# Kernel tuning notes

Measured on AMD Instinct MI355X. Metric: run time of the kernel, lower is better.

## Reference

```python
import jax, jax.numpy as jnp
import numpy as np
import math

B, S, D_MODEL = 4, 2048, 1024
H, D_QK, D_V = 16, 64, 64


def setup_inputs() -> dict:
    key = jax.random.key(0)
    ks = jax.random.split(key, 12)
    s = 0.02
    return {
        "input_q": jax.random.normal(ks[0], (B, S, D_MODEL), jnp.float32),
        "input_k": jax.random.normal(ks[1], (B, S, D_MODEL), jnp.float32),
        "input_v": jax.random.normal(ks[2], (B, S, D_MODEL), jnp.float32),
        # per-head projection weights stacked over heads: [H, out, d_model] (torch Linear layout)
        "WQw": jax.random.normal(ks[3], (H, D_QK, D_MODEL), jnp.float32) * s,
        "WQb": jax.random.normal(ks[4], (H, D_QK), jnp.float32) * s,
        "WKw": jax.random.normal(ks[5], (H, D_QK, D_MODEL), jnp.float32) * s,
        "WKb": jax.random.normal(ks[6], (H, D_QK), jnp.float32) * s,
        "WVw": jax.random.normal(ks[7], (H, D_V, D_MODEL), jnp.float32) * s,
        "WVb": jax.random.normal(ks[8], (H, D_V), jnp.float32) * s,
        # output projection: Linear(H*D_V, D_MODEL)
        "Ww": jax.random.normal(ks[9], (D_MODEL, H * D_V), jnp.float32) * s,
        "Wb": jax.random.normal(ks[10], (D_MODEL,), jnp.float32) * s,
    }


def _mha(input_q, input_k, input_v, WQw, WQb, WKw, WKb, WVw, WVb, Ww, Wb):
    # per-head projections: [B,H,S,d]
    Q = jnp.einsum("bsd,hed->bhse", input_q, WQw) + WQb[None, :, None, :]
    K = jnp.einsum("bsd,hed->bhse", input_k, WKw) + WKb[None, :, None, :]
    V = jnp.einsum("bsd,hvd->bhsv", input_v, WVw) + WVb[None, :, None, :]
    scores = jnp.einsum("bhse,bhte->bhst", Q, K)  # [B,H,S,S]
    # causal mask added BEFORE division by sqrt(d_model), as in original
    causal = jnp.triu(jnp.full((S, S), -jnp.inf, scores.dtype), k=1)
    scores = (scores + causal) / math.sqrt(D_MODEL)  # NOTE: d_model, not d_qk
    attn = jax.nn.softmax(scores, axis=-1)
    ctx = jnp.einsum("bhst,bhtv->bhsv", attn, V)  # [B,H,S,D_V]
    concat = ctx.transpose(0, 2, 1, 3).reshape(B, S, H * D_V)  # head-order concat
    return concat @ Ww.T + Wb


def reference(input_q, input_k, input_v, WQw, WQb, WKw, WKb, WVw, WVb, Ww, Wb):
    return _mha(input_q, input_k, input_v, WQw, WQb, WKw, WKb, WVw, WVb, Ww, Wb)
```

## Files before the change

### kernel.cpp

```cpp
#include <hip/hip_runtime.h>
#include <hip/hip_bf16.h>

typedef __attribute__((ext_vector_type(8))) short bf16x8;
typedef __attribute__((ext_vector_type(4))) short bf16x4;
typedef __attribute__((ext_vector_type(4))) float f32x4;

#define MFMA16(a, b, c) __builtin_amdgcn_mfma_f32_16x16x32_bf16(a, b, c, 0, 0, 0)

__device__ __forceinline__ unsigned short f2bfn(float f) {
#if defined(__gfx950__)
  __bf16 h = (__bf16)f;
  return __builtin_bit_cast(unsigned short, h);
#else
  union { float f; unsigned u; } x; x.f = f;
  unsigned r = x.u + 0x7fffu + ((x.u >> 16) & 1u);
  return (unsigned short)(r >> 16);
#endif
}

__device__ __forceinline__ void cvt_body(const float* __restrict__ s,
                                         unsigned short* __restrict__ d, int n8) {
  int i = blockIdx.x * blockDim.x + threadIdx.x;
  int st = gridDim.x * blockDim.x;
  for (; i < n8; i += st) {
    const float4* sp = reinterpret_cast<const float4*>(s) + 2 * (size_t)i;
    float4 a = sp[0], b = sp[1];
    bf16x8 o;
    o[0] = (short)f2bfn(a.x); o[1] = (short)f2bfn(a.y);
    o[2] = (short)f2bfn(a.z); o[3] = (short)f2bfn(a.w);
    o[4] = (short)f2bfn(b.x); o[5] = (short)f2bfn(b.y);
    o[6] = (short)f2bfn(b.z); o[7] = (short)f2bfn(b.w);
    reinterpret_cast<bf16x8*>(d)[i] = o;
  }
}

__global__ void cvt1_kernel(const float* __restrict__ s, unsigned short* __restrict__ d, int n8) {
  cvt_body(s, d, n8);
}

__global__ void cvt_w_kernel(const float* s0, const float* s1, const float* s2, const float* s3,
                             unsigned short* d0, unsigned short* d1, unsigned short* d2,
                             unsigned short* d3, int n8) {
  const float* s; unsigned short* d;
  switch (blockIdx.y) {
    case 0: s = s0; d = d0; break;
    case 1: s = s1; d = d1; break;
    case 2: s = s2; d = d2; break;
    default: s = s3; d = d3; break;
  }
  cvt_body(s, d, n8);
}

template <int MODE>
__global__ __launch_bounds__(256) void gemm_kernel(
    const unsigned short* __restrict__ Av, const unsigned short* __restrict__ Bv,
    const float* __restrict__ bias, void* __restrict__ outv,
    int M, int N, int K) {
  constexpr int BM = 128, BN = 128, BK = 64;
  __shared__ __align__(16) unsigned short As[2][BM * BK];
  __shared__ __align__(16) unsigned short Bs[2][BN * BK];
  const int tid = threadIdx.x;
  const int lane = tid & 63, wave = tid >> 6;
  const int wr = wave >> 1, wc = wave & 1;
  const int m0 = blockIdx.y * BM, n0 = blockIdx.x * BN;
  const int rb = lane & 15, g = lane >> 4;
  const int swz = ((lane & 7) ^ ((lane >> 3) & 7)) * 8;
  f32x4 acc[4][4] = {};

  const unsigned short* Ab = Av + (size_t)m0 * K;
  const unsigned short* Bb = Bv + (size_t)n0 * K;

  auto stage = [&](int buf, int k0) {
#pragma unroll
    for (int i = 0; i < 4; ++i) {
      const int c = wave * 256 + i * 64 + lane;
      const int r = c >> 3;
      __builtin_amdgcn_global_load_lds(
          (const __attribute__((address_space(1))) unsigned int*)(Ab + (size_t)r * K + k0 + swz),
          (__attribute__((address_space(3))) unsigned int*)&As[buf][c * 8], 16, 0, 0);
      __builtin_amdgcn_global_load_lds(
          (const __attribute__((address_space(1))) unsigned int*)(Bb + (size_t)r * K + k0 + swz),
          (__attribute__((address_space(3))) unsigned int*)&Bs[buf][c * 8], 16, 0, 0);
    }
  };

  const int nt = K / BK;
  stage(0, 0);
  int cur = 0;
  for (int t = 0; t < nt; ++t) {
    __syncthreads();
    if (t + 1 < nt) stage(cur ^ 1, (t + 1) * BK);
    const unsigned short* A_ = As[cur];
    const unsigned short* B_ = Bs[cur];
#pragma unroll
    for (int kc = 0; kc < 2; ++kc) {
      bf16x8 af[4], bfr[4];
#pragma unroll
      for (int mi = 0; mi < 4; ++mi)
        af[mi] = *reinterpret_cast<const bf16x8*>(
            &A_[(wr * 64 + mi * 16 + rb) * 64 + (((kc * 4 + g) ^ (rb & 7)) * 8)]);
#pragma unroll
      for (int ni = 0; ni < 4; ++ni)
        bfr[ni] = *reinterpret_cast<const bf16x8*>(
            &B_[(wc * 64 + ni * 16 + rb) * 64 + (((kc * 4 + g) ^ (rb & 7)) * 8)]);
#pragma unroll
      for (int mi = 0; mi < 4; ++mi)
#pragma unroll
        for (int ni = 0; ni < 4; ++ni)
          acc[mi][ni] = MFMA16(af[mi], bfr[ni], acc[mi][ni]);
    }
    cur ^= 1;
  }

#pragma unroll
  for (int mi = 0; mi < 4; ++mi) {
#pragma unroll
    for (int ni = 0; ni < 4; ++ni) {
      int col = n0 + wc * 64 + ni * 16 + rb;
      if constexpr (MODE != 2) {
        float bv = bias[col];
#pragma unroll
        for (int j = 0; j < 4; ++j) {
          int row = m0 + wr * 64 + mi * 16 + g * 4 + j;
          float v = acc[mi][ni][j] + bv;
          if constexpr (MODE == 0) {
            int b = row >> 11, s = row & 2047;
            int h = col >> 6, e = col & 63;
            ((unsigned short*)outv)[((size_t)(b * 16 + h) * 2048 + s) * 64 + e] = f2bfn(v);
          } else {
            ((float*)outv)[(size_t)row * N + col] = v;
          }
        }
      } else {
        int bb = col >> 11, s = col & 2047;
#pragma unroll
        for (int j = 0; j < 4; ++j) {
          int row = m0 + wr * 64 + mi * 16 + g * 4 + j;
          float v = acc[mi][ni][j] + bias[row];
          int h = row >> 6, e = row & 63;
          ((unsigned short*)outv)[((size_t)(bb * 16 + h) * 64 + e) * 2048 + s] = f2bfn(v);
        }
      }
    }
  }
}

__global__ __launch_bounds__(256) void attn2_kernel(
    const unsigned short* __restrict__ Qp, const unsigned short* __restrict__ Kp,
    const unsigned short* __restrict__ Vtp, unsigned short* __restrict__ ctx) {
  constexpr int S = 2048;
  __shared__ __align__(16) unsigned short Ks[2][64 * 64];
  __shared__ __align__(16) unsigned short Vs[2][64 * 64];
  __shared__ __align__(16) unsigned short Pl[4][32 * 64];
  const int bx = blockIdx.x;
  const int bh = bx & 63;
  const int qti = 15 - (bx >> 6);
  const int q0 = qti * 128;
  const int tid = threadIdx.x, wave = tid >> 6, lane = tid & 63;
  const int q15 = lane & 15, g = lane >> 4;
  const int qw = q0 + wave * 32;
  const unsigned short* Qb = Qp + (size_t)bh * S * 64;
  const unsigned short* Kb = Kp + (size_t)bh * S * 64;
  const unsigned short* Vb = Vtp + (size_t)bh * 64 * S;

  bf16x8 qf[2][2];
#pragma unroll
  for (int ni = 0; ni < 2; ++ni)
#pragma unroll
    for (int kc = 0; kc < 2; ++kc)
      qf[ni][kc] = *reinterpret_cast<const bf16x8*>(
          Qb + (size_t)(qw + 16 * ni + q15) * 64 + 32 * kc + 8 * g);

  float m2[2] = {-1e30f, -1e30f}, nm2[2] = {0.f, 0.f}, lsum[2] = {0.f, 0.f};
  f32x4 o[4][2] = {};
  const float sc = 0.03125f * 1.4426950408889634f;
  const float TH = 8.0f / sc;
  const int xsw = (q15 & 7);
  const int sswz = ((lane & 7) ^ (lane >> 3)) * 8;
  const int nt = qti * 2 + 2;

  auto stage = [&](int buf, int kv0) {
#pragma unroll
    for (int i = 0; i < 2; ++i) {
      const int ci = (wave * 2 + i) * 64 + lane;
      const int r = (wave * 2 + i) * 8 + (lane >> 3);
      const unsigned short* ksrc = Kb + (size_t)(kv0 + r) * 64 + sswz;
      __builtin_amdgcn_global_load_lds(
          (const __attribute__((address_space(1))) unsigned int*)ksrc,
          (__attribute__((address_space(3))) unsigned int*)&Ks[buf][ci * 8], 16, 0, 0);
      const unsigned short* vsrc = Vb + (size_t)r * S + kv0 + sswz;
      __builtin_amdgcn_global_load_lds(
          (const __attribute__((address_space(1))) unsigned int*)vsrc,
          (__attribute__((address_space(3))) unsigned int*)&Vs[buf][ci * 8], 16, 0, 0);
    }
  };

  stage(0, 0);

  for (int it = 0; it < nt; ++it) {
    __syncthreads();
    if (it + 1 < nt) stage((it + 1) & 1, 64 * (it + 1));
    const int kv0 = 64 * it;
    if (kv0 <= qw + 31) {
      const unsigned short* K_ = Ks[it & 1];
      const unsigned short* V_ = Vs[it & 1];
      f32x4 sacc[4][2] = {};
      __builtin_amdgcn_s_setprio(1);
#pragma unroll
      for (int kc = 0; kc < 2; ++kc) {
#pragma unroll
        for (int mi = 0; mi < 4; ++mi) {
          bf16x8 kf = *reinterpret_cast<const bf16x8*>(
              &K_[(16 * mi + q15) * 64 + ((4 * kc + g) ^ xsw) * 8]);
          sacc[mi][0] = MFMA16(kf, qf[0][kc], sacc[mi][0]);
          sacc[mi][1] = MFMA16(kf, qf[1][kc], sacc[mi][1]);
        }
      }
      __builtin_amdgcn_s_setprio(0);
      if (kv0 + 63 > qw) {
#pragma unroll
        for (int mi = 0; mi < 4; ++mi)
#pragma unroll
          for (int ni = 0; ni < 2; ++ni)
#pragma unroll
            for (int j = 0; j < 4; ++j)
              if (kv0 + 16 * mi + 4 * g + j > qw + 16 * ni + q15) sacc[mi][ni][j] = -1e30f;
      }
      float mt[2] = {-1e30f, -1e30f};
#pragma unroll
      for (int mi = 0; mi < 4; ++mi)
#pragma unroll
        for (int ni = 0; ni < 2; ++ni)
#pragma unroll
          for (int j = 0; j < 4; ++j) mt[ni] = fmaxf(mt[ni], sacc[mi][ni][j]);
#pragma unroll
      for (int ni = 0; ni < 2; ++ni) {
        mt[ni] = fmaxf(mt[ni], __shfl_xor(mt[ni], 16, 64));
        mt[ni] = fmaxf(mt[ni], __shfl_xor(mt[ni], 32, 64));
      }
      bool need = (mt[0] > m2[0] + TH) || (mt[1] > m2[1] + TH);
      if (__any((int)need)) {
#pragma unroll
        for (int ni = 0; ni < 2; ++ni) {
          float mn = fmaxf(m2[ni], mt[ni]);
          float corr = __builtin_amdgcn_exp2f((m2[ni] - mn) * sc);
          m2[ni] = mn;
          nm2[ni] = -mn * sc;
          lsum[ni] *= corr;
#pragma unroll
          for (int mi = 0; mi < 4; ++mi)
#pragma unroll
            for (int j = 0; j < 4; ++j) o[mi][ni][j] *= corr;
        }
      }
      float rs[2] = {0.f, 0.f};
#pragma unroll
      for (int mi = 0; mi < 4; ++mi)
#pragma unroll
        for (int ni = 0; ni < 2; ++ni) {
          bf16x4 pk;
#pragma unroll
          for (int j = 0; j < 4; ++j) {
            float p = __builtin_amdgcn_exp2f(fmaf(sacc[mi][ni][j], sc, nm2[ni]));
            rs[ni] += p;
            pk[j] = (short)f2bfn(p);
          }
          *reinterpret_cast<bf16x4*>(
              &Pl[wave][(q15 + 16 * ni) * 64 +
                        ((2 * mi + (g >> 1)) ^ xsw) * 8 + 4 * (g & 1)]) = pk;
        }
#pragma unroll
      for (int ni = 0; ni < 2; ++ni) {
        rs[ni] += __shfl_xor(rs[ni], 16, 64);
        rs[ni] += __shfl_xor(rs[ni], 32, 64);
        lsum[ni] += rs[ni];
      }
      __builtin_amdgcn_s_setprio(1);
#pragma unroll
      for (int kc = 0; kc < 2; ++kc) {
        bf16x8 pf[2];
#pragma unroll
        for (int ni = 0; ni < 2; ++ni)
          pf[ni] = *reinterpret_cast<const bf16x8*>(
              &Pl[wave][(q15 + 16 * ni) * 64 + ((4 * kc + g) ^ xsw) * 8]);
#pragma unroll
        for (int mi = 0; mi < 4; ++mi) {
          bf16x8 vf = *reinterpret_cast<const bf16x8*>(
              &V_[(16 * mi + q15) * 64 + ((4 * kc + g) ^ xsw) * 8]);
          o[mi][0] = MFMA16(vf, pf[0], o[mi][0]);
          o[mi][1] = MFMA16(vf, pf[1], o[mi][1]);
        }
      }
      __builtin_amdgcn_s_setprio(0);
    }
  }

  const int b = bh >> 4, h = bh & 15;
#pragma unroll
  for (int ni = 0; ni < 2; ++ni) {
    float inv = 1.0f / lsum[ni];
    int q = qw + 16 * ni + q15;
#pragma unroll
    for (int mi = 0; mi < 4; ++mi) {
      bf16x4 pk;
#pragma unroll
      for (int j = 0; j < 4; ++j) pk[j] = (short)f2bfn(o[mi][ni][j] * inv);
      *reinterpret_cast<bf16x4*>(
          ctx + ((size_t)(b * 2048 + q) * 1024) + h * 64 + 16 * mi + 4 * g) = pk;
    }
  }
}

extern "C" void kernel_launch(void* const* d_in, const int* in_sizes, int n_in,
                              void* d_out, int out_size, void* d_ws, size_t ws_size,
                              hipStream_t stream) {
  const float* in_q = (const float*)d_in[0];
  const float* in_k = (const float*)d_in[1];
  const float* in_v = (const float*)d_in[2];
  const float* WQw = (const float*)d_in[3];
  const float* WQb = (const float*)d_in[4];
  const float* WKw = (const float*)d_in[5];
  const float* WKb = (const float*)d_in[6];
  const float* WVw = (const float*)d_in[7];
  const float* WVb = (const float*)d_in[8];
  const float* Ww  = (const float*)d_in[9];
  const float* Wb  = (const float*)d_in[10];
  float* out = (float*)d_out;

  constexpr size_t PROJ = (size_t)4 * 16 * 2048 * 64;
  constexpr size_t WSZ = (size_t)1024 * 1024;
  unsigned short* wsp = (unsigned short*)d_ws;
  unsigned short* Qp   = wsp;
  unsigned short* Kp   = wsp + PROJ;
  unsigned short* Vt   = wsp + 2 * PROJ;
  unsigned short* in16 = wsp + 3 * PROJ;
  unsigned short* ctx  = in16;
  unsigned short* wq16 = wsp + 4 * PROJ;
  unsigned short* wk16 = wq16 + WSZ;
  unsigned short* wv16 = wk16 + WSZ;
  unsigned short* ww16 = wv16 + WSZ;

  cvt_w_kernel<<<dim3(256, 4), 256, 0, stream>>>(WQw, WKw, WVw, Ww,
                                                 wq16, wk16, wv16, ww16, (int)(WSZ / 8));
  cvt1_kernel<<<2048, 256, 0, stream>>>(in_q, in16, (int)(PROJ / 8));
  gemm_kernel<0><<<dim3(8, 64), 256, 0, stream>>>(in16, wq16, WQb, Qp, 8192, 1024, 1024);
  cvt1_kernel<<<2048, 256, 0, stream>>>(in_k, in16, (int)(PROJ / 8));
  gemm_kernel<0><<<dim3(8, 64), 256, 0, stream>>>(in16, wk16, WKb, Kp, 8192, 1024, 1024);
  cvt1_kernel<<<2048, 256, 0, stream>>>(in_v, in16, (int)(PROJ / 8));
  gemm_kernel<2><<<dim3(64, 8), 256, 0, stream>>>(wv16, in16, WVb, Vt, 1024, 8192, 1024);

  attn2_kernel<<<1024, 256, 0, stream>>>(Qp, Kp, Vt, ctx);

  gemm_kernel<1><<<dim3(8, 64), 256, 0, stream>>>(ctx, ww16, Wb, out, 8192, 1024, 1024);
}
```

Before: 196.5 us.

## Switch attention to 32x32 MFMA and keep P in registers via permlane swaps

The attention kernel moves from 16x16x32 to 32x32x16 bf16 MFMA tiles, so each wave computes one 32-query block against two 32-key blocks. The softmax probabilities are packed with v_cvt_pk_bf16_f32 and rearranged into the B-operand layout with permlane32_swap, which removes the per-wave LDS round trip for P. Row max and sum reductions now need only one cross-half shuffle. The cost is more live accumulator registers, which may lower occupancy, and a layout correctness that depends on the permlane mapping.

```diff
diff --git a/kernel.cpp b/kernel.cpp
--- a/kernel.cpp
+++ b/kernel.cpp
@@ -4,8 +4,10 @@
 typedef __attribute__((ext_vector_type(8))) short bf16x8;
 typedef __attribute__((ext_vector_type(4))) short bf16x4;
 typedef __attribute__((ext_vector_type(4))) float f32x4;
+typedef __attribute__((ext_vector_type(16))) float f32x16;
 
 #define MFMA16(a, b, c) __builtin_amdgcn_mfma_f32_16x16x32_bf16(a, b, c, 0, 0, 0)
+#define MFMA32(a, b, c) __builtin_amdgcn_mfma_f32_32x32x16_bf16(a, b, c, 0, 0, 0)
 
 __device__ __forceinline__ unsigned short f2bfn(float f) {
 #if defined(__gfx950__)
@@ -16,6 +18,18 @@
   unsigned r = x.u + 0x7fffu + ((x.u >> 16) & 1u);
   return (unsigned short)(r >> 16);
 #endif
+}
+
+__device__ __forceinline__ void plswap(unsigned& a, unsigned& b) {
+  auto r = __builtin_amdgcn_permlane32_swap(a, b, false, false);
+  a = r[0];
+  b = r[1];
+}
+
+__device__ __forceinline__ unsigned cvtpk(float lo, float hi) {
+  unsigned w;
+  asm("v_cvt_pk_bf16_f32 %0, %1, %2" : "=v"(w) : "v"(lo), "v"(hi));
+  return w;
 }
 
 __device__ __forceinline__ void cvt_body(const float* __restrict__ s,
@@ -145,37 +159,34 @@
   }
 }
 
-__global__ __launch_bounds__(256) void attn2_kernel(
+__global__ __launch_bounds__(256) void attn3_kernel(
     const unsigned short* __restrict__ Qp, const unsigned short* __restrict__ Kp,
     const unsigned short* __restrict__ Vtp, unsigned short* __restrict__ ctx) {
   constexpr int S = 2048;
   __shared__ __align__(16) unsigned short Ks[2][64 * 64];
   __shared__ __align__(16) unsigned short Vs[2][64 * 64];
-  __shared__ __align__(16) unsigned short Pl[4][32 * 64];
   const int bx = blockIdx.x;
   const int bh = bx & 63;
   const int qti = 15 - (bx >> 6);
   const int q0 = qti * 128;
   const int tid = threadIdx.x, wave = tid >> 6, lane = tid & 63;
-  const int q15 = lane & 15, g = lane >> 4;
+  const int l31 = lane & 31, hb = lane >> 5, hb4 = hb * 4;
+  const int x7 = l31 & 7;
   const int qw = q0 + wave * 32;
   const unsigned short* Qb = Qp + (size_t)bh * S * 64;
   const unsigned short* Kb = Kp + (size_t)bh * S * 64;
   const unsigned short* Vb = Vtp + (size_t)bh * 64 * S;
 
-  bf16x8 qf[2][2];
-#pragma unroll
-  for (int ni = 0; ni < 2; ++ni)
-#pragma unroll
-    for (int kc = 0; kc < 2; ++kc)
-      qf[ni][kc] = *reinterpret_cast<const bf16x8*>(
-          Qb + (size_t)(qw + 16 * ni + q15) * 64 + 32 * kc + 8 * g);
-
-  float m2[2] = {-1e30f, -1e30f}, nm2[2] = {0.f, 0.f}, lsum[2] = {0.f, 0.f};
-  f32x4 o[4][2] = {};
+  bf16x8 qg[4];
+#pragma unroll
+  for (int kc = 0; kc < 4; ++kc)
+    qg[kc] = *reinterpret_cast<const bf16x8*>(
+        Qb + (size_t)(qw + l31) * 64 + 16 * kc + 8 * hb);
+
+  float m2 = -1e30f, nm2 = 0.f, lsum = 0.f;
+  f32x16 o[2] = {};
   const float sc = 0.03125f * 1.4426950408889634f;
   const float TH = 8.0f / sc;
-  const int xsw = (q15 & 7);
   const int sswz = ((lane & 7) ^ (lane >> 3)) * 8;
   const int nt = qti * 2 + 2;
 
@@ -184,13 +195,11 @@
     for (int i = 0; i < 2; ++i) {
       const int ci = (wave * 2 + i) * 64 + lane;
       const int r = (wave * 2 + i) * 8 + (lane >> 3);
-      const unsigned short* ksrc = Kb + (size_t)(kv0 + r) * 64 + sswz;
       __builtin_amdgcn_global_load_lds(
-          (const __attribute__((address_space(1))) unsigned int*)ksrc,
+          (const __attribute__((address_space(1))) unsigned int*)(Kb + (size_t)(kv0 + r) * 64 + sswz),
           (__attribute__((address_space(3))) unsigned int*)&Ks[buf][ci * 8], 16, 0, 0);
-      const unsigned short* vsrc = Vb + (size_t)r * S + kv0 + sswz;
       __builtin_amdgcn_global_load_lds(
-          (const __attribute__((address_space(1))) unsigned int*)vsrc,
+          (const __attribute__((address_space(1))) unsigned int*)(Vb + (size_t)r * S + kv0 + sswz),
           (__attribute__((address_space(3))) unsigned int*)&Vs[buf][ci * 8], 16, 0, 0);
     }
   };
@@ -204,111 +213,97 @@
     if (kv0 <= qw + 31) {
       const unsigned short* K_ = Ks[it & 1];
       const unsigned short* V_ = Vs[it & 1];
-      f32x4 sacc[4][2] = {};
+      f32x16 sacc[2] = {};
       __builtin_amdgcn_s_setprio(1);
 #pragma unroll
-      for (int kc = 0; kc < 2; ++kc) {
-#pragma unroll
-        for (int mi = 0; mi < 4; ++mi) {
-          bf16x8 kf = *reinterpret_cast<const bf16x8*>(
-              &K_[(16 * mi + q15) * 64 + ((4 * kc + g) ^ xsw) * 8]);
-          sacc[mi][0] = MFMA16(kf, qf[0][kc], sacc[mi][0]);
-          sacc[mi][1] = MFMA16(kf, qf[1][kc], sacc[mi][1]);
-        }
+      for (int kc = 0; kc < 4; ++kc) {
+        bf16x8 kf0 = *reinterpret_cast<const bf16x8*>(
+            &K_[l31 * 64 + ((2 * kc + hb) ^ x7) * 8]);
+        bf16x8 kf1 = *reinterpret_cast<const bf16x8*>(
+            &K_[(32 + l31) * 64 + ((2 * kc + hb) ^ x7) * 8]);
+        sacc[0] = MFMA32(kf0, qg[kc], sacc[0]);
+        sacc[1] = MFMA32(kf1, qg[kc], sacc[1]);
       }
       __builtin_amdgcn_s_setprio(0);
       if (kv0 + 63 > qw) {
-#pragma unroll
-        for (int mi = 0; mi < 4; ++mi)
-#pragma unroll
-          for (int ni = 0; ni < 2; ++ni)
-#pragma unroll
-            for (int j = 0; j < 4; ++j)
-              if (kv0 + 16 * mi + 4 * g + j > qw + 16 * ni + q15) sacc[mi][ni][j] = -1e30f;
-      }
-      float mt[2] = {-1e30f, -1e30f};
-#pragma unroll
-      for (int mi = 0; mi < 4; ++mi)
-#pragma unroll
-        for (int ni = 0; ni < 2; ++ni)
-#pragma unroll
-          for (int j = 0; j < 4; ++j) mt[ni] = fmaxf(mt[ni], sacc[mi][ni][j]);
-#pragma unroll
-      for (int ni = 0; ni < 2; ++ni) {
-        mt[ni] = fmaxf(mt[ni], __shfl_xor(mt[ni], 16, 64));
-        mt[ni] = fmaxf(mt[ni], __shfl_xor(mt[ni], 32, 64));
-      }
-      bool need = (mt[0] > m2[0] + TH) || (mt[1] > m2[1] + TH);
-      if (__any((int)need)) {
-#pragma unroll
-        for (int ni = 0; ni < 2; ++ni) {
-          float mn = fmaxf(m2[ni], mt[ni]);
-          float corr = __builtin_amdgcn_exp2f((m2[ni] - mn) * sc);
-          m2[ni] = mn;
-          nm2[ni] = -mn * sc;
-          lsum[ni] *= corr;
-#pragma unroll
-          for (int mi = 0; mi < 4; ++mi)
-#pragma unroll
-            for (int j = 0; j < 4; ++j) o[mi][ni][j] *= corr;
+        const int qrel = qw + l31 - kv0;
+#pragma unroll
+        for (int mi = 0; mi < 2; ++mi)
+#pragma unroll
+          for (int r = 0; r < 16; ++r) {
+            int koff = 32 * mi + (r & 3) + 8 * (r >> 2) + hb4;
+            if (koff > qrel) sacc[mi][r] = -1e30f;
+          }
+      }
+      float mt = -1e30f;
+#pragma unroll
+      for (int mi = 0; mi < 2; ++mi)
+#pragma unroll
+        for (int r = 0; r < 16; ++r) mt = fmaxf(mt, sacc[mi][r]);
+      mt = fmaxf(mt, __shfl_xor(mt, 32, 64));
+      if (__any((int)(mt > m2 + TH))) {
+        float mn = fmaxf(m2, mt);
+        float corr = __builtin_amdgcn_exp2f((m2 - mn) * sc);
+        m2 = mn; nm2 = -mn * sc;
+        lsum *= corr;
+#pragma unroll
+        for (int db = 0; db < 2; ++db)
+#pragma unroll
+          for (int r = 0; r < 16; ++r) o[db][r] *= corr;
+      }
+      float rs = 0.f;
+      unsigned pw[2][8];
+#pragma unroll
+      for (int mi = 0; mi < 2; ++mi) {
+        float p[16];
+#pragma unroll
+        for (int r = 0; r < 16; ++r) {
+          p[r] = __builtin_amdgcn_exp2f(fmaf(sacc[mi][r], sc, nm2));
+          rs += p[r];
         }
-      }
-      float rs[2] = {0.f, 0.f};
-#pragma unroll
-      for (int mi = 0; mi < 4; ++mi)
-#pragma unroll
-        for (int ni = 0; ni < 2; ++ni) {
-          bf16x4 pk;
-#pragma unroll
-          for (int j = 0; j < 4; ++j) {
-            float p = __builtin_amdgcn_exp2f(fmaf(sacc[mi][ni][j], sc, nm2[ni]));
-            rs[ni] += p;
-            pk[j] = (short)f2bfn(p);
-          }
-          *reinterpret_cast<bf16x4*>(
-              &Pl[wave][(q15 + 16 * ni) * 64 +
-                        ((2 * mi + (g >> 1)) ^ xsw) * 8 + 4 * (g & 1)]) = pk;
+#pragma unroll
+        for (int i = 0; i < 8; ++i) pw[mi][i] = cvtpk(p[2 * i], p[2 * i + 1]);
+      }
+      lsum += rs;
+#pragma unroll
+      for (int mi = 0; mi < 2; ++mi) {
+        plswap(pw[mi][0], pw[mi][2]);
+        plswap(pw[mi][1], pw[mi][3]);
+        plswap(pw[mi][4], pw[mi][6]);
+        plswap(pw[mi][5], pw[mi][7]);
+      }
+      __builtin_amdgcn_s_setprio(1);
+#pragma unroll
+      for (int c = 0; c < 4; ++c) {
+        union { unsigned u[4]; bf16x8 v; } pu;
+        pu.u[0] = pw[c >> 1][(c & 1) * 4 + 0];
+        pu.u[1] = pw[c >> 1][(c & 1) * 4 + 1];
+        pu.u[2] = pw[c >> 1][(c & 1) * 4 + 2];
+        pu.u[3] = pw[c >> 1][(c & 1) * 4 + 3];
+#pragma unroll
+        for (int db = 0; db < 2; ++db) {
+          bf16x8 vf = *reinterpret_cast<const bf16x8*>(
+              &V_[(32 * db + l31) * 64 + ((2 * c + hb) ^ x7) * 8]);
+          o[db] = MFMA32(vf, pu.v, o[db]);
         }
-#pragma unroll
-      for (int ni = 0; ni < 2; ++ni) {
-        rs[ni] += __shfl_xor(rs[ni], 16, 64);
-        rs[ni] += __shfl_xor(rs[ni], 32, 64);
-        lsum[ni] += rs[ni];
-      }
-      __builtin_amdgcn_s_setprio(1);
-#pragma unroll
-      for (int kc = 0; kc < 2; ++kc) {
-        bf16x8 pf[2];
-#pragma unroll
-        for (int ni = 0; ni < 2; ++ni)
-          pf[ni] = *reinterpret_cast<const bf16x8*>(
-              &Pl[wave][(q15 + 16 * ni) * 64 + ((4 * kc + g) ^ xsw) * 8]);
-#pragma unroll
-        for (int mi = 0; mi < 4; ++mi) {
-          bf16x8 vf = *reinterpret_cast<const bf16x8*>(
-              &V_[(16 * mi + q15) * 64 + ((4 * kc + g) ^ xsw) * 8]);
-          o[mi][0] = MFMA16(vf, pf[0], o[mi][0]);
-          o[mi][1] = MFMA16(vf, pf[1], o[mi][1]);
-        }
       }
       __builtin_amdgcn_s_setprio(0);
     }
   }
 
+  const float tot = lsum + __shfl_xor(lsum, 32, 64);
+  const float inv = 1.0f / tot;
   const int b = bh >> 4, h = bh & 15;
-#pragma unroll
-  for (int ni = 0; ni < 2; ++ni) {
-    float inv = 1.0f / lsum[ni];
-    int q = qw + 16 * ni + q15;
-#pragma unroll
-    for (int mi = 0; mi < 4; ++mi) {
-      bf16x4 pk;
-#pragma unroll
-      for (int j = 0; j < 4; ++j) pk[j] = (short)f2bfn(o[mi][ni][j] * inv);
-      *reinterpret_cast<bf16x4*>(
-          ctx + ((size_t)(b * 2048 + q) * 1024) + h * 64 + 16 * mi + 4 * g) = pk;
-    }
-  }
+  const int q = qw + l31;
+  unsigned short* cp = ctx + ((size_t)(b * 2048 + q) * 1024) + h * 64;
+#pragma unroll
+  for (int db = 0; db < 2; ++db)
+#pragma unroll
+    for (int i = 0; i < 8; ++i) {
+      unsigned w = cvtpk(o[db][2 * i] * inv, o[db][2 * i + 1] * inv);
+      int d = 32 * db + ((2 * i) & 3) + 8 * (i >> 1) + hb4;
+      *reinterpret_cast<unsigned*>(cp + d) = w;
+    }
 }
 
 extern "C" void kernel_launch(void* const* d_in, const int* in_sizes, int n_in,
@@ -349,7 +344,7 @@
   cvt1_kernel<<<2048, 256, 0, stream>>>(in_v, in16, (int)(PROJ / 8));
   gemm_kernel<2><<<dim3(64, 8), 256, 0, stream>>>(wv16, in16, WVb, Vt, 1024, 8192, 1024);
 
-  attn2_kernel<<<1024, 256, 0, stream>>>(Qp, Kp, Vt, ctx);
+  attn3_kernel<<<1024, 256, 0, stream>>>(Qp, Kp, Vt, ctx);
 
   gemm_kernel<1><<<dim3(8, 64), 256, 0, stream>>>(ctx, ww16, Wb, out, 8192, 1024, 1024);
 }
```

Measured after the change: 192.5 us. 1.02x faster.
